# Optimization experiments

Hardware: AMD Instinct MI355X
Metric: run time of the kernel (lower is better)

Reference implementation:

```python
import jax, jax.numpy as jnp
import numpy as np

N = 50000
E = 300000
D_IN = 128
H = 256
D_OUT = 256


def _glorot(key, shape):
    fan_in, fan_out = shape[0], shape[1]
    lim = float(np.sqrt(6.0 / (fan_in + fan_out)))
    return jax.random.uniform(key, shape, jnp.float32, -lim, lim)


def setup_inputs() -> dict:
    key = jax.random.key(0)
    ks = jax.random.split(key, 12)
    x = jax.random.normal(ks[0], (N, D_IN), jnp.float32)
    edge_index = jax.random.randint(ks[1], (2, E), 0, N, jnp.int64)
    return {
        "x": x,
        "edge_index": edge_index,
        "W1": _glorot(ks[2], (D_IN, H)),  "b1": jnp.zeros((H,), jnp.float32),
        "Wg1": _glorot(ks[3], (H, H)),    "bg1": jnp.zeros((H,), jnp.float32),
        "Wg2": _glorot(ks[4], (H, H)),    "bg2": jnp.zeros((H,), jnp.float32),
        "W2": _glorot(ks[5], (H, H)),     "b2": jnp.zeros((H,), jnp.float32),
        "W3": _glorot(ks[6], (H, D_OUT)), "b3": jnp.zeros((D_OUT,), jnp.float32),
    }


def _gcn_conv(h, src, dst, W, b):
    # PyG GCNConv: h' = D^-1/2 (A + I) D^-1/2 (h W) + b, deg counted at target with self-loops
    h = h @ W                                           # [N, H]
    deg = jnp.zeros((N,), h.dtype).at[dst].add(1.0) + 1.0
    dinv = jax.lax.rsqrt(deg)                           # deg^-1/2, [N]
    norm = dinv[src] * dinv[dst]                        # [E]
    msg = h[src] * norm[:, None]                        # gather + scale, [E, H]
    agg = jax.ops.segment_sum(msg, dst, num_segments=N)  # scatter-add
    agg = agg + h * (dinv * dinv)[:, None]              # self-loop contribution (norm = 1/deg)
    return agg + b


def reference(x, edge_index, W1, b1, Wg1, bg1, Wg2, bg2, W2, b2, W3, b3):
    src, dst = edge_index[0], edge_index[1]
    h = jax.nn.relu(x @ W1 + b1)
    h = jax.nn.relu(_gcn_conv(h, src, dst, Wg1, bg1))
    h = jax.nn.relu(_gcn_conv(h, src, dst, Wg2, bg2))
    h = jax.nn.relu(h @ W2 + b2)
    return jax.nn.softmax(h @ W3 + b3, axis=1)
```

## Files before the change

### kernel.cpp

```cpp
#include <hip/hip_runtime.h>
#include <math.h>

#define HDIM 256

typedef float floatx4 __attribute__((ext_vector_type(4)));
typedef __bf16 bf16x8 __attribute__((ext_vector_type(8)));
typedef unsigned short ushortx4 __attribute__((ext_vector_type(4)));

#define AS1C(p) ((const __attribute__((address_space(1))) void*)(p))
#define AS3(p)  ((__attribute__((address_space(3))) void*)(p))

__device__ inline unsigned short bf16_rn(float f) {
  unsigned u = __float_as_uint(f);
  return (unsigned short)((u + 0x7FFFu + ((u >> 16) & 1u)) >> 16);
}

__device__ inline void split_f32(float f, unsigned short& h, unsigned short& l) {
  unsigned short hb = bf16_rn(f);
  float hf = __uint_as_float(((unsigned)hb) << 16);
  h = hb;
  l = bf16_rn(f - hf);
}


__global__ __launch_bounds__(256)
void prep_w_staged(const float* __restrict__ W, unsigned short* __restrict__ SH,
                   unsigned short* __restrict__ SL, int K) {
  int idx = blockIdx.x * 256 + threadIdx.x;
  int total = K * 32;
  if (idx >= total) return;
  int chunksPerCb = total >> 1;
  int cb = (idx >= chunksPerCb) ? 1 : 0;
  int rem = idx - cb * chunksPerCb;
  int kt = rem >> 9;
  int chunk = rem & 511;
  int kc = chunk >> 7;
  int col = chunk & 127;
  const float* src = W + (size_t)(kt * 32 + kc * 8) * HDIM + cb * 128 + col;
#pragma unroll
  for (int e = 0; e < 8; ++e) {
    unsigned short h, l;
    split_f32(src[(size_t)e * HDIM], h, l);
    SH[(size_t)idx * 8 + e] = h;
    SL[(size_t)idx * 8 + e] = l;
  }
}


__global__ __launch_bounds__(256)
void deg_count_kernel(const int* __restrict__ ei, int* __restrict__ deg, int E) {
  int e = blockIdx.x * 256 + threadIdx.x;
  if (e < E) atomicAdd(&deg[ei[E + e]], 1);
}

__global__ __launch_bounds__(256)
void dinv_kernel(const int* __restrict__ deg, float* __restrict__ dinv, int n) {
  int i = blockIdx.x * 256 + threadIdx.x;
  if (i < n) dinv[i] = 1.0f / sqrtf((float)deg[i] + 1.0f);
}

__global__ __launch_bounds__(256)
void block_sum_kernel(const int* __restrict__ deg, int* __restrict__ bsum, int n) {
  __shared__ int sm[256];
  int t = threadIdx.x;
  int idx = blockIdx.x * 256 + t;
  sm[t] = (idx < n) ? deg[idx] : 0;
  __syncthreads();
  for (int off = 128; off > 0; off >>= 1) {
    if (t < off) sm[t] += sm[t + off];
    __syncthreads();
  }
  if (t == 0) bsum[blockIdx.x] = sm[0];
}

__global__ __launch_bounds__(256)
void scan_bsums_kernel(const int* __restrict__ bsum, int* __restrict__ boff,
                       int* __restrict__ rowptr, int nb, int n) {
  __shared__ int sm[256];
  int t = threadIdx.x;
  int v = (t < nb) ? bsum[t] : 0;
  sm[t] = v;
  __syncthreads();
  for (int off = 1; off < 256; off <<= 1) {
    int a = (t >= off) ? sm[t - off] : 0;
    __syncthreads();
    sm[t] += a;
    __syncthreads();
  }
  if (t < nb) boff[t] = sm[t] - v;
  if (t == 255) rowptr[n] = sm[255];
}

__global__ __launch_bounds__(256)
void scan_final_kernel(const int* __restrict__ deg, const int* __restrict__ boff,
                       int* __restrict__ rowptr, int* __restrict__ cursor, int n) {
  __shared__ int sm[256];
  int t = threadIdx.x;
  int idx = blockIdx.x * 256 + t;
  int v = (idx < n) ? deg[idx] : 0;
  sm[t] = v;
  __syncthreads();
  for (int off = 1; off < 256; off <<= 1) {
    int a = (t >= off) ? sm[t - off] : 0;
    __syncthreads();
    sm[t] += a;
    __syncthreads();
  }
  int excl = sm[t] - v + boff[blockIdx.x];
  if (idx < n) { rowptr[idx] = excl; cursor[idx] = excl; }
}

__global__ __launch_bounds__(256)
void fill_csr_kernel(const int* __restrict__ ei, int* __restrict__ cursor,
                     int* __restrict__ col, int E) {
  int e = blockIdx.x * 256 + threadIdx.x;
  if (e < E) {
    int s = ei[e];
    int d = ei[E + e];
    int p = atomicAdd(&cursor[d], 1);
    col[p] = s;
  }
}


template<bool BIAS, bool RELU>
__global__ __launch_bounds__(256, 3)
void mfma_gemm_splitA(const float* __restrict__ A,
                      const unsigned short* __restrict__ SWH,
                      const unsigned short* __restrict__ SWL,
                      const float* __restrict__ bias,
                      unsigned short* __restrict__ CH, unsigned short* __restrict__ CL,
                      int M, int K) {
  __shared__ __align__(16) unsigned short AsH[128 * 40];
  __shared__ __align__(16) unsigned short AsL[128 * 40];
  __shared__ __align__(16) unsigned short BsH[4096];
  __shared__ __align__(16) unsigned short BsL[4096];

  const int tid = threadIdx.x;
  const int w = tid >> 6;
  const int l = tid & 63;
  const int l15 = l & 15;
  const int quad = l >> 4;
  const int wm = w & 1;
  const int wn = w >> 1;
  const int bm = blockIdx.y * 128;
  const int bn = blockIdx.x * 128;
  const int ktc = K >> 5;

  floatx4 acc[4][4];
#pragma unroll
  for (int i = 0; i < 4; ++i)
#pragma unroll
    for (int j = 0; j < 4; ++j) acc[i][j] = (floatx4){0.f, 0.f, 0.f, 0.f};

  for (int kt = 0; kt < ktc; ++kt) {
    int k0 = kt * 32;
    float4 av[4];
#pragma unroll
    for (int i = 0; i < 4; ++i) {
      int chunk = i * 256 + tid;
      int row = chunk >> 3;
      int kc4 = chunk & 7;
      int grow = bm + row;
      if (grow > M - 1) grow = M - 1;
      av[i] = *(const float4*)(A + (size_t)grow * K + k0 + kc4 * 4);
    }

    __syncthreads();

    size_t wb = ((size_t)(blockIdx.x * ktc + kt)) * 4096;
#pragma unroll
    for (int j = 0; j < 2; ++j) {
      int c = j * 256 + tid;
      __builtin_amdgcn_global_load_lds(AS1C(SWH + wb + (size_t)c * 8),
                                       AS3(&BsH[(j * 256 + w * 64) * 8]), 16, 0, 0);
      __builtin_amdgcn_global_load_lds(AS1C(SWL + wb + (size_t)c * 8),
                                       AS3(&BsL[(j * 256 + w * 64) * 8]), 16, 0, 0);
    }

#pragma unroll
    for (int i = 0; i < 4; ++i) {
      int chunk = i * 256 + tid;
      int row = chunk >> 3;
      int kc4 = chunk & 7;
      unsigned short h0, h1, h2, h3, l0, l1, l2, l3;
      split_f32(av[i].x, h0, l0);
      split_f32(av[i].y, h1, l1);
      split_f32(av[i].z, h2, l2);
      split_f32(av[i].w, h3, l3);
      *(ushortx4*)&AsH[row * 40 + kc4 * 4] = (ushortx4){h0, h1, h2, h3};
      *(ushortx4*)&AsL[row * 40 + kc4 * 4] = (ushortx4){l0, l1, l2, l3};
    }

    __syncthreads();

    bf16x8 aH[4], aL[4];
#pragma unroll
    for (int fi = 0; fi < 4; ++fi) {
      int row = wm * 64 + fi * 16 + l15;
      aH[fi] = *(const bf16x8*)&AsH[row * 40 + quad * 8];
      aL[fi] = *(const bf16x8*)&AsL[row * 40 + quad * 8];
    }
#pragma unroll
    for (int fj = 0; fj < 4; ++fj) {
      int colL = wn * 64 + fj * 16 + l15;
      int cidx = quad * 128 + colL;
      bf16x8 bh = *(const bf16x8*)&BsH[cidx * 8];
      bf16x8 bl = *(const bf16x8*)&BsL[cidx * 8];
#pragma unroll
      for (int fi = 0; fi < 4; ++fi) {
        floatx4 t = acc[fi][fj];
        t = __builtin_amdgcn_mfma_f32_16x16x32_bf16(aH[fi], bl, t, 0, 0, 0);
        t = __builtin_amdgcn_mfma_f32_16x16x32_bf16(aL[fi], bh, t, 0, 0, 0);
        t = __builtin_amdgcn_mfma_f32_16x16x32_bf16(aH[fi], bh, t, 0, 0, 0);
        acc[fi][fj] = t;
      }
    }
  }

  float bcol[4];
#pragma unroll
  for (int fj = 0; fj < 4; ++fj)
    bcol[fj] = BIAS ? bias[bn + wn * 64 + fj * 16 + l15] : 0.f;

#pragma unroll
  for (int fi = 0; fi < 4; ++fi) {
    int rb = bm + wm * 64 + fi * 16 + quad * 4;
#pragma unroll
    for (int r = 0; r < 4; ++r) {
      int row = rb + r;
      if (row < M) {
        size_t base = (size_t)row * HDIM + bn + wn * 64 + l15;
#pragma unroll
        for (int fj = 0; fj < 4; ++fj) {
          float v = acc[fi][fj][r] + bcol[fj];
          if (RELU) v = fmaxf(v, 0.f);
          unsigned short h, lo;
          split_f32(v, h, lo);
          CH[base + fj * 16] = h;
          CL[base + fj * 16] = lo;
        }
      }
    }
  }
}


template<bool BIAS, bool RELU, bool SPLIT_OUT>
__global__ __launch_bounds__(256, 3)
void mfma_gemm_p(const unsigned short* __restrict__ AH, const unsigned short* __restrict__ AL,
                 const unsigned short* __restrict__ SWH, const unsigned short* __restrict__ SWL,
                 const float* __restrict__ bias,
                 float* __restrict__ C, unsigned short* __restrict__ CH,
                 unsigned short* __restrict__ CL, int M, int K) {
  __shared__ __align__(16) unsigned short AsH[4096];
  __shared__ __align__(16) unsigned short AsL[4096];
  __shared__ __align__(16) unsigned short BsH[4096];
  __shared__ __align__(16) unsigned short BsL[4096];

  const int tid = threadIdx.x;
  const int w = tid >> 6;
  const int l = tid & 63;
  const int l15 = l & 15;
  const int quad = l >> 4;
  const int wm = w & 1;
  const int wn = w >> 1;
  const int bm = blockIdx.y * 128;
  const int bn = blockIdx.x * 128;
  const int ktc = K >> 5;

  floatx4 acc[4][4];
#pragma unroll
  for (int i = 0; i < 4; ++i)
#pragma unroll
    for (int j = 0; j < 4; ++j) acc[i][j] = (floatx4){0.f, 0.f, 0.f, 0.f};

  for (int kt = 0; kt < ktc; ++kt) {
    __syncthreads();

#pragma unroll
    for (int i = 0; i < 2; ++i) {
      int L = i * 256 + tid;
      int row = L >> 2;
      int p = L & 3;
      int kc = p ^ (row & 3) ^ ((row >> 2) & 3);
      int grow = bm + row;
      if (grow > M - 1) grow = M - 1;
      const unsigned short* gH = AH + (size_t)grow * K + kt * 32 + kc * 8;
      const unsigned short* gL = AL + (size_t)grow * K + kt * 32 + kc * 8;
      __builtin_amdgcn_global_load_lds(AS1C(gH), AS3(&AsH[(i * 256 + w * 64) * 8]), 16, 0, 0);
      __builtin_amdgcn_global_load_lds(AS1C(gL), AS3(&AsL[(i * 256 + w * 64) * 8]), 16, 0, 0);
    }
    size_t wb = ((size_t)(blockIdx.x * ktc + kt)) * 4096;
#pragma unroll
    for (int j = 0; j < 2; ++j) {
      int c = j * 256 + tid;
      __builtin_amdgcn_global_load_lds(AS1C(SWH + wb + (size_t)c * 8),
                                       AS3(&BsH[(j * 256 + w * 64) * 8]), 16, 0, 0);
      __builtin_amdgcn_global_load_lds(AS1C(SWL + wb + (size_t)c * 8),
                                       AS3(&BsL[(j * 256 + w * 64) * 8]), 16, 0, 0);
    }

    __syncthreads();

    bf16x8 aH[4], aL[4];
#pragma unroll
    for (int fi = 0; fi < 4; ++fi) {
      int r = wm * 64 + fi * 16 + l15;
      int sw = quad ^ (r & 3) ^ ((r >> 2) & 3);
      aH[fi] = *(const bf16x8*)&AsH[(r * 4 + sw) * 8];
      aL[fi] = *(const bf16x8*)&AsL[(r * 4 + sw) * 8];
    }
#pragma unroll
    for (int fj = 0; fj < 4; ++fj) {
      int colL = wn * 64 + fj * 16 + l15;
      int cidx = quad * 128 + colL;
      bf16x8 bh = *(const bf16x8*)&BsH[cidx * 8];
      bf16x8 bl = *(const bf16x8*)&BsL[cidx * 8];
#pragma unroll
      for (int fi = 0; fi < 4; ++fi) {
        floatx4 t = acc[fi][fj];
        t = __builtin_amdgcn_mfma_f32_16x16x32_bf16(aH[fi], bl, t, 0, 0, 0);
        t = __builtin_amdgcn_mfma_f32_16x16x32_bf16(aL[fi], bh, t, 0, 0, 0);
        t = __builtin_amdgcn_mfma_f32_16x16x32_bf16(aH[fi], bh, t, 0, 0, 0);
        acc[fi][fj] = t;
      }
    }
  }

  float bcol[4];
#pragma unroll
  for (int fj = 0; fj < 4; ++fj)
    bcol[fj] = BIAS ? bias[bn + wn * 64 + fj * 16 + l15] : 0.f;

#pragma unroll
  for (int fi = 0; fi < 4; ++fi) {
    int rb = bm + wm * 64 + fi * 16 + quad * 4;
#pragma unroll
    for (int r = 0; r < 4; ++r) {
      int row = rb + r;
      if (row < M) {
        size_t base = (size_t)row * HDIM + bn + wn * 64 + l15;
        if (SPLIT_OUT) {
#pragma unroll
          for (int fj = 0; fj < 4; ++fj) {
            float v = acc[fi][fj][r] + bcol[fj];
            if (RELU) v = fmaxf(v, 0.f);
            unsigned short h, lo;
            split_f32(v, h, lo);
            CH[base + fj * 16] = h;
            CL[base + fj * 16] = lo;
          }
        } else {
#pragma unroll
          for (int fj = 0; fj < 4; ++fj) {
            float v = acc[fi][fj][r] + bcol[fj];
            if (RELU) v = fmaxf(v, 0.f);
            C[base + fj * 16] = v;
          }
        }
      }
    }
  }
}


__global__ __launch_bounds__(512, 4)
void mfma_gemm_softmax(const unsigned short* __restrict__ AH, const unsigned short* __restrict__ AL,
                       const unsigned short* __restrict__ SWH, const unsigned short* __restrict__ SWL,
                       const float* __restrict__ bias, float* __restrict__ out, int M, int K) {
  __shared__ __align__(16) unsigned short AsH[4096];
  __shared__ __align__(16) unsigned short AsL[4096];
  __shared__ __align__(16) unsigned short BsH[8192];
  __shared__ __align__(16) unsigned short BsL[8192];
  __shared__ float smax[128 * 4];
  __shared__ float ssum[128 * 4];

  const int tid = threadIdx.x;
  const int w = tid >> 6;
  const int l = tid & 63;
  const int l15 = l & 15;
  const int quad = l >> 4;
  const int wm = w & 1;
  const int wn = w >> 1;
  const int bm = blockIdx.x * 128;
  const int ktc = K >> 5;
  const int chunksPerCb = ktc * 512;

  floatx4 acc[4][4];
#pragma unroll
  for (int i = 0; i < 4; ++i)
#pragma unroll
    for (int j = 0; j < 4; ++j) acc[i][j] = (floatx4){0.f, 0.f, 0.f, 0.f};

  for (int kt = 0; kt < ktc; ++kt) {
    __syncthreads();

    {
      int L = tid;
      int row = L >> 2;
      int p = L & 3;
      int kc = p ^ (row & 3) ^ ((row >> 2) & 3);
      int grow = bm + row;
      if (grow > M - 1) grow = M - 1;
      const unsigned short* gH = AH + (size_t)grow * K + kt * 32 + kc * 8;
      const unsigned short* gL = AL + (size_t)grow * K + kt * 32 + kc * 8;
      __builtin_amdgcn_global_load_lds(AS1C(gH), AS3(&AsH[(w * 64) * 8]), 16, 0, 0);
      __builtin_amdgcn_global_load_lds(AS1C(gL), AS3(&AsL[(w * 64) * 8]), 16, 0, 0);
    }
#pragma unroll
    for (int j = 0; j < 2; ++j) {
      int pos = j * 512 + w * 64 + l;
      int kc = pos >> 8;
      int within = pos & 255;
      int cb = within >> 7;
      int colL = within & 127;
      size_t gi = (size_t)cb * chunksPerCb + (size_t)kt * 512 + kc * 128 + colL;
      __builtin_amdgcn_global_load_lds(AS1C(SWH + gi * 8),
                                       AS3(&BsH[(j * 512 + w * 64) * 8]), 16, 0, 0);
      __builtin_amdgcn_global_load_lds(AS1C(SWL + gi * 8),
                                       AS3(&BsL[(j * 512 + w * 64) * 8]), 16, 0, 0);
    }

    __syncthreads();

    bf16x8 aH[4], aL[4];
#pragma unroll
    for (int fi = 0; fi < 4; ++fi) {
      int r = wm * 64 + fi * 16 + l15;
      int sw = quad ^ (r & 3) ^ ((r >> 2) & 3);
      aH[fi] = *(const bf16x8*)&AsH[(r * 4 + sw) * 8];
      aL[fi] = *(const bf16x8*)&AsL[(r * 4 + sw) * 8];
    }
#pragma unroll
    for (int fj = 0; fj < 4; ++fj) {
      int colG = wn * 64 + fj * 16 + l15;
      int cidx = quad * 256 + colG;
      bf16x8 bh = *(const bf16x8*)&BsH[cidx * 8];
      bf16x8 bl = *(const bf16x8*)&BsL[cidx * 8];
#pragma unroll
      for (int fi = 0; fi < 4; ++fi) {
        floatx4 t = acc[fi][fj];
        t = __builtin_amdgcn_mfma_f32_16x16x32_bf16(aH[fi], bl, t, 0, 0, 0);
        t = __builtin_amdgcn_mfma_f32_16x16x32_bf16(aL[fi], bh, t, 0, 0, 0);
        t = __builtin_amdgcn_mfma_f32_16x16x32_bf16(aH[fi], bh, t, 0, 0, 0);
        acc[fi][fj] = t;
      }
    }
  }

  float bcol[4];
#pragma unroll
  for (int fj = 0; fj < 4; ++fj)
    bcol[fj] = bias[wn * 64 + fj * 16 + l15];

#pragma unroll
  for (int fi = 0; fi < 4; ++fi) {
#pragma unroll
    for (int r = 0; r < 4; ++r) {
      float mv = -3.4e38f;
#pragma unroll
      for (int fj = 0; fj < 4; ++fj) mv = fmaxf(mv, acc[fi][fj][r] + bcol[fj]);
#pragma unroll
      for (int off = 1; off < 16; off <<= 1) mv = fmaxf(mv, __shfl_xor(mv, off));
      int row = wm * 64 + fi * 16 + quad * 4 + r;
      if (l15 == 0) smax[row * 4 + wn] = mv;
    }
  }
  __syncthreads();

#pragma unroll
  for (int fi = 0; fi < 4; ++fi) {
#pragma unroll
    for (int r = 0; r < 4; ++r) {
      int row = wm * 64 + fi * 16 + quad * 4 + r;
      float gm = fmaxf(fmaxf(smax[row * 4 + 0], smax[row * 4 + 1]),
                       fmaxf(smax[row * 4 + 2], smax[row * 4 + 3]));
      float s = 0.f;
#pragma unroll
      for (int fj = 0; fj < 4; ++fj) {
        float p = expf(acc[fi][fj][r] + bcol[fj] - gm);
        acc[fi][fj][r] = p;
        s += p;
      }
#pragma unroll
      for (int off = 1; off < 16; off <<= 1) s += __shfl_xor(s, off);
      if (l15 == 0) ssum[row * 4 + wn] = s;
    }
  }
  __syncthreads();

#pragma unroll
  for (int fi = 0; fi < 4; ++fi) {
#pragma unroll
    for (int r = 0; r < 4; ++r) {
      int row = wm * 64 + fi * 16 + quad * 4 + r;
      int grow = bm + row;
      if (grow < M) {
        float inv = 1.0f / (ssum[row * 4 + 0] + ssum[row * 4 + 1] +
                            ssum[row * 4 + 2] + ssum[row * 4 + 3]);
        float* Cp = out + (size_t)grow * HDIM + wn * 64 + l15;
#pragma unroll
        for (int fj = 0; fj < 4; ++fj) Cp[fj * 16] = acc[fi][fj][r] * inv;
      }
    }
  }
}


__global__ __launch_bounds__(256)
void aggregate_b(const float* __restrict__ t, const float* __restrict__ dinv,
                 const int* __restrict__ rowptr, const int* __restrict__ col,
                 const float* __restrict__ bias,
                 unsigned short* __restrict__ OH, unsigned short* __restrict__ OL, int n) {
  int gw = (int)((blockIdx.x * 256 + threadIdx.x) >> 6);
  int lane = threadIdx.x & 63;
  if (gw >= n) return;
  float di = dinv[gw];
  float4 v = ((const float4*)(t + (size_t)gw * HDIM))[lane];
  float ss = di * di;
  float a0 = v.x * ss, a1 = v.y * ss, a2 = v.z * ss, a3 = v.w * ss;
  int e0 = rowptr[gw], e1 = rowptr[gw + 1];

  for (int base = e0; base < e1; base += 8) {
    int cs[8];
#pragma unroll
    for (int i = 0; i < 8; ++i) {
      int e = base + i;
      if (e > e1 - 1) e = e1 - 1;
      cs[i] = col[e];
    }
    float wg[8];
#pragma unroll
    for (int i = 0; i < 8; ++i)
      wg[i] = (base + i < e1) ? dinv[cs[i]] * di : 0.f;
    float4 rw[8];
#pragma unroll
    for (int i = 0; i < 8; ++i)
      rw[i] = ((const float4*)(t + (size_t)cs[i] * HDIM))[lane];
#pragma unroll
    for (int i = 0; i < 8; ++i) {
      a0 = fmaf(rw[i].x, wg[i], a0);
      a1 = fmaf(rw[i].y, wg[i], a1);
      a2 = fmaf(rw[i].z, wg[i], a2);
      a3 = fmaf(rw[i].w, wg[i], a3);
    }
  }

  float4 bb = ((const float4*)bias)[lane];
  float r0 = fmaxf(a0 + bb.x, 0.f);
  float r1 = fmaxf(a1 + bb.y, 0.f);
  float r2 = fmaxf(a2 + bb.z, 0.f);
  float r3 = fmaxf(a3 + bb.w, 0.f);
  unsigned short h0, h1, h2, h3, l0, l1, l2, l3;
  split_f32(r0, h0, l0);
  split_f32(r1, h1, l1);
  split_f32(r2, h2, l2);
  split_f32(r3, h3, l3);
  ((ushortx4*)(OH + (size_t)gw * HDIM))[lane] = (ushortx4){h0, h1, h2, h3};
  ((ushortx4*)(OL + (size_t)gw * HDIM))[lane] = (ushortx4){l0, l1, l2, l3};
}


extern "C" void kernel_launch(void* const* d_in, const int* in_sizes, int n_in,
                              void* d_out, int out_size, void* d_ws, size_t ws_size,
                              hipStream_t stream) {
  const float* x   = (const float*)d_in[0];
  const int*   ei  = (const int*)d_in[1];
  const float* W1  = (const float*)d_in[2];
  const float* b1  = (const float*)d_in[3];
  const float* Wg1 = (const float*)d_in[4];
  const float* bg1 = (const float*)d_in[5];
  const float* Wg2 = (const float*)d_in[6];
  const float* bg2 = (const float*)d_in[7];
  const float* W2  = (const float*)d_in[8];
  const float* b2  = (const float*)d_in[9];
  const float* W3  = (const float*)d_in[10];
  const float* b3  = (const float*)d_in[11];
  float* out = (float*)d_out;

  const int K1 = in_sizes[2] / HDIM;
  const int N  = in_sizes[0] / K1;
  const int E  = in_sizes[1] / 2;

  char* w = (char*)d_ws;
  auto alloc = [&](size_t bytes) -> char* {
    char* p = w;
    w += (bytes + 255) & ~(size_t)255;
    return p;
  };
  unsigned short* PH = (unsigned short*)alloc((size_t)N * HDIM * 2);
  unsigned short* PL = (unsigned short*)alloc((size_t)N * HDIM * 2);
  float* dinv   = (float*)alloc((size_t)N * sizeof(float));
  int*   deg    = (int*)alloc((size_t)N * sizeof(int));
  int*   rowptr = (int*)alloc((size_t)(N + 1) * sizeof(int));
  int*   cursor = (int*)alloc((size_t)N * sizeof(int));
  int*   col    = (int*)alloc((size_t)E * sizeof(int));
  const int nb  = (N + 255) / 256;
  int*   bsum   = (int*)alloc((size_t)nb * sizeof(int));
  int*   boff   = (int*)alloc((size_t)nb * sizeof(int));
  unsigned short* W1sH  = (unsigned short*)alloc((size_t)HDIM * K1 * 2);
  unsigned short* W1sL  = (unsigned short*)alloc((size_t)HDIM * K1 * 2);
  unsigned short* Wg1sH = (unsigned short*)alloc((size_t)HDIM * HDIM * 2);
  unsigned short* Wg1sL = (unsigned short*)alloc((size_t)HDIM * HDIM * 2);
  unsigned short* Wg2sH = (unsigned short*)alloc((size_t)HDIM * HDIM * 2);
  unsigned short* Wg2sL = (unsigned short*)alloc((size_t)HDIM * HDIM * 2);
  unsigned short* W2sH  = (unsigned short*)alloc((size_t)HDIM * HDIM * 2);
  unsigned short* W2sL  = (unsigned short*)alloc((size_t)HDIM * HDIM * 2);
  unsigned short* W3sH  = (unsigned short*)alloc((size_t)HDIM * HDIM * 2);
  unsigned short* W3sL  = (unsigned short*)alloc((size_t)HDIM * HDIM * 2);

  unsigned short* QH = (unsigned short*)out;
  unsigned short* QL = QH + (size_t)N * HDIM;

  const int ge = (E + 255) / 256;
  const int gn = (N + 255) / 256;

  prep_w_staged<<<(K1 * 32 + 255) / 256, 256, 0, stream>>>(W1, W1sH, W1sL, K1);
  prep_w_staged<<<(HDIM * 32 + 255) / 256, 256, 0, stream>>>(Wg1, Wg1sH, Wg1sL, HDIM);
  prep_w_staged<<<(HDIM * 32 + 255) / 256, 256, 0, stream>>>(Wg2, Wg2sH, Wg2sL, HDIM);
  prep_w_staged<<<(HDIM * 32 + 255) / 256, 256, 0, stream>>>(W2, W2sH, W2sL, HDIM);
  prep_w_staged<<<(HDIM * 32 + 255) / 256, 256, 0, stream>>>(W3, W3sH, W3sL, HDIM);

  hipMemsetAsync(deg, 0, (size_t)N * sizeof(int), stream);
  deg_count_kernel<<<ge, 256, 0, stream>>>(ei, deg, E);
  dinv_kernel<<<gn, 256, 0, stream>>>(deg, dinv, N);
  block_sum_kernel<<<nb, 256, 0, stream>>>(deg, bsum, N);
  scan_bsums_kernel<<<1, 256, 0, stream>>>(bsum, boff, rowptr, nb, N);
  scan_final_kernel<<<nb, 256, 0, stream>>>(deg, boff, rowptr, cursor, N);
  fill_csr_kernel<<<ge, 256, 0, stream>>>(ei, cursor, col, E);

  dim3 ggrid(2, (N + 127) / 128);
  const int gagg = (N + 3) / 4;
  const int gfuse = (N + 127) / 128;

  mfma_gemm_splitA<true, true><<<ggrid, 256, 0, stream>>>(x, W1sH, W1sL, b1, PH, PL, N, K1);
  mfma_gemm_p<false, false, false><<<ggrid, 256, 0, stream>>>(PH, PL, Wg1sH, Wg1sL, nullptr, out, nullptr, nullptr, N, HDIM);
  aggregate_b<<<gagg, 256, 0, stream>>>(out, dinv, rowptr, col, bg1, PH, PL, N);
  mfma_gemm_p<false, false, false><<<ggrid, 256, 0, stream>>>(PH, PL, Wg2sH, Wg2sL, nullptr, out, nullptr, nullptr, N, HDIM);
  aggregate_b<<<gagg, 256, 0, stream>>>(out, dinv, rowptr, col, bg2, PH, PL, N);
  mfma_gemm_p<true, true, true><<<ggrid, 256, 0, stream>>>(PH, PL, W2sH, W2sL, b2, nullptr, QH, QL, N, HDIM);
  mfma_gemm_softmax<<<gfuse, 512, 0, stream>>>(QH, QL, W3sH, W3sL, b3, out, N, HDIM);
}
```

Baseline: 425.4 us.

## Double-buffer LDS tiles in hidden GEMMs to overlap loads with MFMA

Replaces the single-buffered GEMM for the 256-wide hidden layers with a double-buffered version. The next K tile is issued via global_load_lds while the current tile is computed, with explicit vmcnt waits and barriers. K is fixed at 256 so the loop fully unrolls and address math is hoisted. LDS use doubles and launch bounds drop to 2 blocks per CU, trading occupancy for in-block latency hiding.

Result: no change. 427.2 us (+0.4%).

```diff
diff --git a/kernel.cpp b/kernel.cpp
--- a/kernel.cpp
+++ b/kernel.cpp
@@ -247,16 +247,16 @@
 
 
 template<bool BIAS, bool RELU, bool SPLIT_OUT>
-__global__ __launch_bounds__(256, 3)
-void mfma_gemm_p(const unsigned short* __restrict__ AH, const unsigned short* __restrict__ AL,
-                 const unsigned short* __restrict__ SWH, const unsigned short* __restrict__ SWL,
-                 const float* __restrict__ bias,
-                 float* __restrict__ C, unsigned short* __restrict__ CH,
-                 unsigned short* __restrict__ CL, int M, int K) {
-  __shared__ __align__(16) unsigned short AsH[4096];
-  __shared__ __align__(16) unsigned short AsL[4096];
-  __shared__ __align__(16) unsigned short BsH[4096];
-  __shared__ __align__(16) unsigned short BsL[4096];
+__global__ __launch_bounds__(256, 2)
+void mfma_gemm_pp(const unsigned short* __restrict__ AH, const unsigned short* __restrict__ AL,
+                  const unsigned short* __restrict__ SWH, const unsigned short* __restrict__ SWL,
+                  const float* __restrict__ bias,
+                  float* __restrict__ C, unsigned short* __restrict__ CH,
+                  unsigned short* __restrict__ CL, int M) {
+  __shared__ __align__(16) unsigned short AsH[2][4096];
+  __shared__ __align__(16) unsigned short AsL[2][4096];
+  __shared__ __align__(16) unsigned short BsH[2][4096];
+  __shared__ __align__(16) unsigned short BsL[2][4096];
 
   const int tid = threadIdx.x;
   const int w = tid >> 6;
@@ -266,57 +266,89 @@
   const int wm = w & 1;
   const int wn = w >> 1;
   const int bm = blockIdx.y * 128;
-  const int bn = blockIdx.x * 128;
-  const int ktc = K >> 5;
-
-  floatx4 acc[4][4];
-#pragma unroll
-  for (int i = 0; i < 4; ++i)
-#pragma unroll
-    for (int j = 0; j < 4; ++j) acc[i][j] = (floatx4){0.f, 0.f, 0.f, 0.f};
-
-  for (int kt = 0; kt < ktc; ++kt) {
-    __syncthreads();
-
-#pragma unroll
-    for (int i = 0; i < 2; ++i) {
-      int L = i * 256 + tid;
-      int row = L >> 2;
-      int p = L & 3;
-      int kc = p ^ (row & 3) ^ ((row >> 2) & 3);
-      int grow = bm + row;
-      if (grow > M - 1) grow = M - 1;
-      const unsigned short* gH = AH + (size_t)grow * K + kt * 32 + kc * 8;
-      const unsigned short* gL = AL + (size_t)grow * K + kt * 32 + kc * 8;
-      __builtin_amdgcn_global_load_lds(AS1C(gH), AS3(&AsH[(i * 256 + w * 64) * 8]), 16, 0, 0);
-      __builtin_amdgcn_global_load_lds(AS1C(gL), AS3(&AsL[(i * 256 + w * 64) * 8]), 16, 0, 0);
-    }
-    size_t wb = ((size_t)(blockIdx.x * ktc + kt)) * 4096;
+
+  const unsigned short* gA_H[2];
+  const unsigned short* gA_L[2];
+  int ldsA[2];
+#pragma unroll
+  for (int i = 0; i < 2; ++i) {
+    int L = i * 256 + tid;
+    int row = L >> 2;
+    int p = L & 3;
+    int kc = p ^ (row & 3) ^ ((row >> 2) & 3);
+    int grow = bm + row;
+    if (grow > M - 1) grow = M - 1;
+    gA_H[i] = AH + (size_t)grow * HDIM + kc * 8;
+    gA_L[i] = AL + (size_t)grow * HDIM + kc * 8;
+    ldsA[i] = (i * 256 + w * 64) * 8;
+  }
+  const unsigned short* gB_H[2];
+  const unsigned short* gB_L[2];
+  int ldsB[2];
+  {
+    size_t wb = (size_t)blockIdx.x * 8 * 4096;
 #pragma unroll
     for (int j = 0; j < 2; ++j) {
       int c = j * 256 + tid;
-      __builtin_amdgcn_global_load_lds(AS1C(SWH + wb + (size_t)c * 8),
-                                       AS3(&BsH[(j * 256 + w * 64) * 8]), 16, 0, 0);
-      __builtin_amdgcn_global_load_lds(AS1C(SWL + wb + (size_t)c * 8),
-                                       AS3(&BsL[(j * 256 + w * 64) * 8]), 16, 0, 0);
-    }
-
-    __syncthreads();
+      gB_H[j] = SWH + wb + (size_t)c * 8;
+      gB_L[j] = SWL + wb + (size_t)c * 8;
+      ldsB[j] = (j * 256 + w * 64) * 8;
+    }
+  }
+
+  floatx4 acc[4][4];
+#pragma unroll
+  for (int i = 0; i < 4; ++i)
+#pragma unroll
+    for (int j = 0; j < 4; ++j) acc[i][j] = (floatx4){0.f, 0.f, 0.f, 0.f};
+
+  int aOff[4];
+#pragma unroll
+  for (int fi = 0; fi < 4; ++fi) {
+    int r = wm * 64 + fi * 16 + l15;
+    int sw = quad ^ (r & 3) ^ ((r >> 2) & 3);
+    aOff[fi] = (r * 4 + sw) * 8;
+  }
+
+  auto issue = [&](int kt, int b) {
+#pragma unroll
+    for (int i = 0; i < 2; ++i) {
+      __builtin_amdgcn_global_load_lds(AS1C(gA_H[i] + kt * 32), AS3(&AsH[b][ldsA[i]]), 16, 0, 0);
+      __builtin_amdgcn_global_load_lds(AS1C(gA_L[i] + kt * 32), AS3(&AsL[b][ldsA[i]]), 16, 0, 0);
+    }
+#pragma unroll
+    for (int j = 0; j < 2; ++j) {
+      __builtin_amdgcn_global_load_lds(AS1C(gB_H[j] + (size_t)kt * 4096), AS3(&BsH[b][ldsB[j]]), 16, 0, 0);
+      __builtin_amdgcn_global_load_lds(AS1C(gB_L[j] + (size_t)kt * 4096), AS3(&BsL[b][ldsB[j]]), 16, 0, 0);
+    }
+  };
+
+  issue(0, 0);
+
+#pragma unroll
+  for (int kt = 0; kt < 8; ++kt) {
+    const int cur = kt & 1;
+    __builtin_amdgcn_s_barrier();
+    if (kt < 7) {
+      issue(kt + 1, cur ^ 1);
+      __builtin_amdgcn_s_waitcnt(0xF78);
+    } else {
+      __builtin_amdgcn_s_waitcnt(0xF70);
+    }
+    __builtin_amdgcn_s_barrier();
 
     bf16x8 aH[4], aL[4];
 #pragma unroll
     for (int fi = 0; fi < 4; ++fi) {
-      int r = wm * 64 + fi * 16 + l15;
-      int sw = quad ^ (r & 3) ^ ((r >> 2) & 3);
-      aH[fi] = *(const bf16x8*)&AsH[(r * 4 + sw) * 8];
-      aL[fi] = *(const bf16x8*)&AsL[(r * 4 + sw) * 8];
+      aH[fi] = *(const bf16x8*)&AsH[cur][aOff[fi]];
+      aL[fi] = *(const bf16x8*)&AsL[cur][aOff[fi]];
     }
 #pragma unroll
     for (int fj = 0; fj < 4; ++fj) {
       int colL = wn * 64 + fj * 16 + l15;
       int cidx = quad * 128 + colL;
-      bf16x8 bh = *(const bf16x8*)&BsH[cidx * 8];
-      bf16x8 bl = *(const bf16x8*)&BsL[cidx * 8];
+      bf16x8 bh = *(const bf16x8*)&BsH[cur][cidx * 8];
+      bf16x8 bl = *(const bf16x8*)&BsL[cur][cidx * 8];
 #pragma unroll
       for (int fi = 0; fi < 4; ++fi) {
         floatx4 t = acc[fi][fj];
@@ -328,6 +360,7 @@
     }
   }
 
+  const int bn = blockIdx.x * 128;
   float bcol[4];
 #pragma unroll
   for (int fj = 0; fj < 4; ++fj)
@@ -635,10 +668,10 @@
   const int gfuse = (N + 127) / 128;
 
   mfma_gemm_splitA<true, true><<<ggrid, 256, 0, stream>>>(x, W1sH, W1sL, b1, PH, PL, N, K1);
-  mfma_gemm_p<false, false, false><<<ggrid, 256, 0, stream>>>(PH, PL, Wg1sH, Wg1sL, nullptr, out, nullptr, nullptr, N, HDIM);
+  mfma_gemm_pp<false, false, false><<<ggrid, 256, 0, stream>>>(PH, PL, Wg1sH, Wg1sL, nullptr, out, nullptr, nullptr, N);
   aggregate_b<<<gagg, 256, 0, stream>>>(out, dinv, rowptr, col, bg1, PH, PL, N);
-  mfma_gemm_p<false, false, false><<<ggrid, 256, 0, stream>>>(PH, PL, Wg2sH, Wg2sL, nullptr, out, nullptr, nullptr, N, HDIM);
+  mfma_gemm_pp<false, false, false><<<ggrid, 256, 0, stream>>>(PH, PL, Wg2sH, Wg2sL, nullptr, out, nullptr, nullptr, N);
   aggregate_b<<<gagg, 256, 0, stream>>>(out, dinv, rowptr, col, bg2, PH, PL, N);
-  mfma_gemm_p<true, true, true><<<ggrid, 256, 0, stream>>>(PH, PL, W2sH, W2sL, b2, nullptr, QH, QL, N, HDIM);
+  mfma_gemm_pp<true, true, true><<<ggrid, 256, 0, stream>>>(PH, PL, W2sH, W2sL, b2, nullptr, QH, QL, N);
   mfma_gemm_softmax<<<gfuse, 512, 0, stream>>>(QH, QL, W3sH, W3sL, b3, out, N, HDIM);
 }
```
